# Performance work log

Hardware: AMD Instinct MI355X
Metric: run time of the kernel (lower is better)

Reference implementation:

```python
import jax, jax.numpy as jnp
import numpy as np

DT = 1.0 / 256.0
N = int(1.0 / DT)          # 256
T = 2 * N                   # 512 timeline points
INF = jnp.inf


def _constants(dtype):
    timeline = jnp.arange(T, dtype=dtype) * DT                      # [T], t in [0, 2)
    timeline_rev = jnp.arange(T, 0, -1).astype(dtype)               # [T], descending weights
    thresh = jnp.concatenate([
        jnp.full((N,), INF, dtype=dtype),
        jnp.flip(jnp.arange(N, dtype=dtype)) * DT,                  # (1-dt) ... 0
    ])                                                               # [T]
    return timeline, timeline_rev, thresh


def _mlp_ops(ti, W, timeline, timeline_rev, thresh):
    # ti: [B, I] spike times, 1.0 means no spike -> inf
    ti = jnp.where(ti == 1.0, INF, ti)
    # relu(TimeLine - ti): [B, I, T] piecewise-linear rising voltage per input neuron
    tmp = jax.nn.relu(timeline[None, None, :] - ti[:, :, None])
    # voltage_relay: [B, O, T]
    mem = jnp.einsum('bit,oi->bot', tmp, W)
    vb = (mem > thresh[None, None, :]).astype(mem.dtype)            # [B, O, T]
    last = vb[:, :, -1]                                              # did it ever cross by t_end
    vb = vb.at[:, :, -1].set(1.0)                                    # sentinel so argmax is defined
    first_idx = jnp.argmax(vb * timeline_rev[None, None, :], axis=2) # first crossing index
    spike_time = first_idx.astype(mem.dtype) * DT - 1.0              # map second half -> [0,1)
    spike_time = jnp.where(last == 0.0, 1.0, spike_time)             # nonspike -> 1.0
    return spike_time                                                # [B, O]


def _mlp_ops_last(ti, W):
    # ti: [B, H]; W: [C, H]. Scan t from 1.0 to <5.0 step DT, record first-spike time.
    ti = jnp.where(ti == 1.0, INF, ti)
    n_steps = int(np.ceil(4.0 / DT))                                 # 1024
    ts = 1.0 + DT * jnp.arange(n_steps, dtype=ti.dtype)
    spike0 = jnp.full((ti.shape[0], W.shape[0]), INF, dtype=ti.dtype)
    nonspike_mask = (ti == INF)

    def step(spike_time, t):
        diff = jnp.where(nonspike_mask, 0.0, t - ti)                 # [B, H]
        v = diff @ W.T                                               # [B, C]
        fire = (v > 20.0) & (spike_time == INF)
        spike_time = jnp.where(fire, t, spike_time)
        return spike_time, None

    spike_time, _ = jax.lax.scan(step, spike0, ts)
    return spike_time                                                # [B, C]


def setup_inputs() -> dict:
    key = jax.random.key(0)
    k1, k2, k3 = jax.random.split(key, 3)
    x = jax.random.uniform(k1, (128, 800), dtype=jnp.float32)        # spike times in [0,1)
    W1 = jax.random.normal(k2, (128, 800), dtype=jnp.float32) * 0.05
    W2 = jax.random.normal(k3, (10, 128), dtype=jnp.float32) * 0.05
    return {"x": x, "W1": W1, "W2": W2}


def reference(x, W1, W2):
    timeline, timeline_rev, thresh = _constants(x.dtype)
    h = _mlp_ops(x.reshape(x.shape[0], -1), W1, timeline, timeline_rev, thresh)
    out = _mlp_ops_last(h, W2)
    return out
```

## Files before the change

### kernel.cpp

```cpp
#include <hip/hip_runtime.h>
#include <math.h>


#define DT (1.0f / 256.0f)
#define NSTEP 256
#define TSTEPS 512
#define IN_DIM 800
#define HID 128
#define OUT_DIM 10
#define NOSPIKE 1e30f

__global__ __launch_bounds__(256) void spike_hidden(
    const float* __restrict__ x,
    const float* __restrict__ W1,
    float* __restrict__ hs_out)
{
    const int b   = blockIdx.x >> 3;
    const int q   = blockIdx.x & 7;
    const int tid = threadIdx.x;
    const int n   = q * 16 + (tid >> 4);
    const int s   = tid & 15;

    __shared__ float xm[IN_DIM];
    __shared__ float mk[IN_DIM];

    const float* xr = x + (size_t)b * IN_DIM;
    for (int i = tid; i < IN_DIM; i += 256) {
        float xi = xr[i];
        float m  = (xi != 1.0f) ? 1.0f : 0.0f;
        xm[i] = m * xi;
        mk[i] = m;
    }
    __syncthreads();

    const float* wr = W1 + (size_t)n * IN_DIM;
    float S = 0.0f;
    float A = 0.0f;
#pragma unroll
    for (int k = 0; k < 12; ++k) {
        const int i = k * 64 + s * 4;
        float4 wv = *(const float4*)(wr + i);
        float4 xv = *(const float4*)(&xm[i]);
        float4 mv = *(const float4*)(&mk[i]);
        S = fmaf(mv.x, wv.x, S);  A = fmaf(xv.x, wv.x, A);
        S = fmaf(mv.y, wv.y, S);  A = fmaf(xv.y, wv.y, A);
        S = fmaf(mv.z, wv.z, S);  A = fmaf(xv.z, wv.z, A);
        S = fmaf(mv.w, wv.w, S);  A = fmaf(xv.w, wv.w, A);
    }
    if (s < 8) {
        const int i = 768 + s * 4;
        float4 wv = *(const float4*)(wr + i);
        float4 xv = *(const float4*)(&xm[i]);
        float4 mv = *(const float4*)(&mk[i]);
        S = fmaf(mv.x, wv.x, S);  A = fmaf(xv.x, wv.x, A);
        S = fmaf(mv.y, wv.y, S);  A = fmaf(xv.y, wv.y, A);
        S = fmaf(mv.z, wv.z, S);  A = fmaf(xv.z, wv.z, A);
        S = fmaf(mv.w, wv.w, S);  A = fmaf(xv.w, wv.w, A);
    }
    S += __shfl_xor(S, 1);  A += __shfl_xor(A, 1);
    S += __shfl_xor(S, 2);  A += __shfl_xor(A, 2);
    S += __shfl_xor(S, 4);  A += __shfl_xor(A, 4);
    S += __shfl_xor(S, 8);  A += __shfl_xor(A, 8);

    if (s == 0) {
        float h;
        float mem_last = fmaf(511.0f * DT, S, -A);
        if (!(mem_last > 0.0f)) {
            h = 1.0f;
        } else {
            float Sp = S + 1.0f;
            int tf;
            if (!(Sp > 0.0f)) {
                tf = NSTEP;
            } else {
                float X = (A + 511.0f * DT) / (DT * Sp);
                tf = (int)floorf(X) + 1;
                if (tf < NSTEP)      tf = NSTEP;
                if (tf > TSTEPS - 1) tf = TSTEPS - 1;
            }
            h = (float)tf * DT - 1.0f;
        }
        hs_out[b * HID + n] = h;
    }
}

__global__ __launch_bounds__(640) void spike_out(
    const float* __restrict__ hs,
    const float* __restrict__ W2,
    float* __restrict__ out)
{
    const int b   = blockIdx.x;
    const int tid = threadIdx.x;
    const int o   = tid >> 6;
    const int j   = tid & 63;

    const float* hr = hs + (size_t)b * HID;
    const float* w2 = W2 + (size_t)o * HID;

    float S2 = 0.0f, A2 = 0.0f;
#pragma unroll
    for (int i = j; i < HID; i += 64) {
        float hi = hr[i];
        float w  = w2[i];
        float m  = (hi != 1.0f) ? 1.0f : 0.0f;
        S2 = fmaf(m, w, S2);
        A2 = fmaf(m * hi, w, A2);
    }
#pragma unroll
    for (int msk = 1; msk < 64; msk <<= 1) {
        S2 += __shfl_xor(S2, msk);
        A2 += __shfl_xor(A2, msk);
    }
    if (j == 0) {
        float res = NOSPIKE;
        float v_lo = fmaf(1.0f,                S2, -A2);
        float v_hi = fmaf(1.0f + 1023.0f * DT, S2, -A2);
        if (fmaxf(v_lo, v_hi) > 19.999f) {
            for (int k = 0; k < 1024; ++k) {
                float t = fmaf((float)k, DT, 1.0f);
                float v = fmaf(t, S2, -A2);
                if (v > 20.0f) { res = t; break; }
            }
        }
        out[b * OUT_DIM + o] = res;
    }
}

extern "C" void kernel_launch(void* const* d_in, const int* in_sizes, int n_in,
                              void* d_out, int out_size, void* d_ws, size_t ws_size,
                              hipStream_t stream) {
    const float* x  = (const float*)d_in[0];
    const float* W1 = (const float*)d_in[1];
    const float* W2 = (const float*)d_in[2];
    float* out = (float*)d_out;
    float* hs  = (float*)d_ws;

    spike_hidden<<<1024, 256, 0, stream>>>(x, W1, hs);
    spike_out<<<128, 640, 0, stream>>>(hs, W2, out);
}
```

Measured before the change: 61.97 us.

## Fuse hidden and output spike kernels into one per-batch block

The two kernels are merged into one launch with a 1024-thread block per batch row. That block computes all 128 hidden spike times, keeps them in shared memory and then runs the output layer. This removes the second launch and the global round trip of the hidden activations. In exchange the grid shrinks from 1024 blocks to 128, so the W1 reads (each block streams the whole W1) have less parallelism spread across the GPU's compute units, which may leave many of them idle.

```diff
diff --git a/kernel.cpp b/kernel.cpp
--- a/kernel.cpp
+++ b/kernel.cpp
@@ -10,26 +10,36 @@
 #define OUT_DIM 10
 #define NOSPIKE 1e30f
 
-__global__ __launch_bounds__(256) void spike_hidden(
+__global__ __launch_bounds__(1024) void spike_fused(
     const float* __restrict__ x,
     const float* __restrict__ W1,
-    float* __restrict__ hs_out)
+    const float* __restrict__ W2,
+    float* __restrict__ out)
 {
-    const int b   = blockIdx.x >> 3;
-    const int q   = blockIdx.x & 7;
+    const int b   = blockIdx.x;
     const int tid = threadIdx.x;
-    const int n   = q * 16 + (tid >> 4);
-    const int s   = tid & 15;
+    const int n   = tid >> 3;
+    const int s   = tid & 7;
 
-    __shared__ float xm[IN_DIM];
-    __shared__ float mk[IN_DIM];
+    __shared__ __align__(16) float xm[IN_DIM];
+    __shared__ __align__(16) float mk[IN_DIM];
+    __shared__ float hs_sh[HID];
+
+    float w2a = 0.0f, w2b = 0.0f;
+    if (tid < 640) {
+        const int o = tid >> 6;
+        const int j = tid & 63;
+        const float* w2 = W2 + (size_t)o * HID;
+        w2a = w2[j];
+        w2b = w2[j + 64];
+    }
 
     const float* xr = x + (size_t)b * IN_DIM;
-    for (int i = tid; i < IN_DIM; i += 256) {
-        float xi = xr[i];
+    if (tid < IN_DIM) {
+        float xi = xr[tid];
         float m  = (xi != 1.0f) ? 1.0f : 0.0f;
-        xm[i] = m * xi;
-        mk[i] = m;
+        xm[tid] = m * xi;
+        mk[tid] = m;
     }
     __syncthreads();
 
@@ -37,18 +47,8 @@
     float S = 0.0f;
     float A = 0.0f;
 #pragma unroll
-    for (int k = 0; k < 12; ++k) {
-        const int i = k * 64 + s * 4;
-        float4 wv = *(const float4*)(wr + i);
-        float4 xv = *(const float4*)(&xm[i]);
-        float4 mv = *(const float4*)(&mk[i]);
-        S = fmaf(mv.x, wv.x, S);  A = fmaf(xv.x, wv.x, A);
-        S = fmaf(mv.y, wv.y, S);  A = fmaf(xv.y, wv.y, A);
-        S = fmaf(mv.z, wv.z, S);  A = fmaf(xv.z, wv.z, A);
-        S = fmaf(mv.w, wv.w, S);  A = fmaf(xv.w, wv.w, A);
-    }
-    if (s < 8) {
-        const int i = 768 + s * 4;
+    for (int k = 0; k < 25; ++k) {
+        const int i = k * 32 + s * 4;
         float4 wv = *(const float4*)(wr + i);
         float4 xv = *(const float4*)(&xm[i]);
         float4 mv = *(const float4*)(&mk[i]);
@@ -60,7 +60,6 @@
     S += __shfl_xor(S, 1);  A += __shfl_xor(A, 1);
     S += __shfl_xor(S, 2);  A += __shfl_xor(A, 2);
     S += __shfl_xor(S, 4);  A += __shfl_xor(A, 4);
-    S += __shfl_xor(S, 8);  A += __shfl_xor(A, 8);
 
     if (s == 0) {
         float h;
@@ -80,49 +79,41 @@
             }
             h = (float)tf * DT - 1.0f;
         }
-        hs_out[b * HID + n] = h;
+        hs_sh[n] = h;
     }
-}
+    __syncthreads();
 
-__global__ __launch_bounds__(640) void spike_out(
-    const float* __restrict__ hs,
-    const float* __restrict__ W2,
-    float* __restrict__ out)
-{
-    const int b   = blockIdx.x;
-    const int tid = threadIdx.x;
-    const int o   = tid >> 6;
-    const int j   = tid & 63;
+    if (tid < 640) {
+        const int j = tid & 63;
 
-    const float* hr = hs + (size_t)b * HID;
-    const float* w2 = W2 + (size_t)o * HID;
+        float hi0 = hs_sh[j];
+        float hi1 = hs_sh[j + 64];
+        float m0  = (hi0 != 1.0f) ? 1.0f : 0.0f;
+        float m1  = (hi1 != 1.0f) ? 1.0f : 0.0f;
 
-    float S2 = 0.0f, A2 = 0.0f;
+        float S2 = 0.0f, A2 = 0.0f;
+        S2 = fmaf(m0, w2a, S2);   A2 = fmaf(m0 * hi0, w2a, A2);
+        S2 = fmaf(m1, w2b, S2);   A2 = fmaf(m1 * hi1, w2b, A2);
+
 #pragma unroll
-    for (int i = j; i < HID; i += 64) {
-        float hi = hr[i];
-        float w  = w2[i];
-        float m  = (hi != 1.0f) ? 1.0f : 0.0f;
-        S2 = fmaf(m, w, S2);
-        A2 = fmaf(m * hi, w, A2);
-    }
-#pragma unroll
-    for (int msk = 1; msk < 64; msk <<= 1) {
-        S2 += __shfl_xor(S2, msk);
-        A2 += __shfl_xor(A2, msk);
-    }
-    if (j == 0) {
-        float res = NOSPIKE;
-        float v_lo = fmaf(1.0f,                S2, -A2);
-        float v_hi = fmaf(1.0f + 1023.0f * DT, S2, -A2);
-        if (fmaxf(v_lo, v_hi) > 19.999f) {
-            for (int k = 0; k < 1024; ++k) {
-                float t = fmaf((float)k, DT, 1.0f);
-                float v = fmaf(t, S2, -A2);
-                if (v > 20.0f) { res = t; break; }
+        for (int msk = 1; msk < 64; msk <<= 1) {
+            S2 += __shfl_xor(S2, msk);
+            A2 += __shfl_xor(A2, msk);
+        }
+        if (j == 0) {
+            const int o = tid >> 6;
+            float res = NOSPIKE;
+            float v_lo = fmaf(1.0f,                S2, -A2);
+            float v_hi = fmaf(1.0f + 1023.0f * DT, S2, -A2);
+            if (fmaxf(v_lo, v_hi) > 19.999f) {
+                for (int k = 0; k < 1024; ++k) {
+                    float t = fmaf((float)k, DT, 1.0f);
+                    float v = fmaf(t, S2, -A2);
+                    if (v > 20.0f) { res = t; break; }
+                }
             }
+            out[b * OUT_DIM + o] = res;
         }
-        out[b * OUT_DIM + o] = res;
     }
 }
 
@@ -133,8 +124,7 @@
     const float* W1 = (const float*)d_in[1];
     const float* W2 = (const float*)d_in[2];
     float* out = (float*)d_out;
-    float* hs  = (float*)d_ws;
+    (void)d_ws; (void)ws_size;
 
-    spike_hidden<<<1024, 256, 0, stream>>>(x, W1, hs);
-    spike_out<<<128, 640, 0, stream>>>(hs, W2, out);
+    spike_fused<<<128, 1024, 0, stream>>>(x, W1, W2, out);
 }
```

Measured after the change: 61.18 us. About the same (-1.3%).
